# Performance work log

Measured on AMD Instinct MI355X. Metric: run time of the kernel, lower is better.

## Reference

```python
import jax, jax.numpy as jnp
import numpy as np
from jax import lax

N_ANT = 16
T_SNAP = 512
M_SRC = 3
BATCH = 1024
N_ANGLES = 360


def setup_inputs() -> dict:
    key = jax.random.key(0)
    ks = jax.random.split(key, 16)
    H = 2 * N_ANT  # GRU input/hidden size
    p = lambda k, shp, s=0.05: jax.random.normal(k, shp, jnp.float32) * s
    return {
        "X_real": jax.random.normal(ks[0], (BATCH, N_ANT, T_SNAP), jnp.float32),
        "X_imag": jax.random.normal(ks[1], (BATCH, N_ANT, T_SNAP), jnp.float32),
        "bn_w": jnp.ones((T_SNAP,), jnp.float32),
        "bn_b": jnp.zeros((T_SNAP,), jnp.float32),
        "gru_Wih": p(ks[2], (3 * H, H), 0.1),
        "gru_Whh": p(ks[3], (3 * H, H), 0.1),
        "gru_bih": p(ks[4], (3 * H,), 0.1),
        "gru_bhh": p(ks[5], (3 * H,), 0.1),
        "fc_W": p(ks[6], (H * N_ANT, H)),
        "fc_b": p(ks[7], (H * N_ANT,)),
        "fc1_W": p(ks[8], (H, N_ANGLES)),
        "fc1_b": p(ks[9], (H,)),
        "fc2_W": p(ks[10], (H, H)),
        "fc2_b": p(ks[11], (H,)),
        "fc3_W": p(ks[12], (M_SRC, H)),
        "fc3_b": p(ks[13], (M_SRC,)),
    }


def _gru_last(x, Wih, Whh, bih, bhh):
    # x: [B, T, I]; torch GRU gate order: r, z, n. Returns last hidden state [B, H].
    B = x.shape[0]
    H = Whh.shape[1]

    def step(h, xt):
        gi = xt @ Wih.T + bih
        gh = h @ Whh.T + bhh
        ir, iz, inn = jnp.split(gi, 3, axis=-1)
        hr, hz, hn = jnp.split(gh, 3, axis=-1)
        r = jax.nn.sigmoid(ir + hr)
        z = jax.nn.sigmoid(iz + hz)
        n = jnp.tanh(inn + r * hn)
        h_new = (1.0 - z) * n + z * h
        return h_new, None

    h0 = jnp.zeros((B, H), x.dtype)
    hT, _ = lax.scan(step, h0, jnp.swapaxes(x, 0, 1))
    return hT


def reference(X_real, X_imag, bn_w, bn_b, gru_Wih, gru_Whh, gru_bih, gru_bhh,
              fc_W, fc_b, fc1_W, fc1_b, fc2_W, fc2_b, fc3_W, fc3_b):
    B, N, T = X_real.shape
    # cat(real, imag) on antenna dim -> [B, 2N, T], then raw view to [B, T, 2N] (faithful to .view)
    X = jnp.concatenate([X_real, X_imag], axis=1).reshape(B, T, 2 * N)
    # BatchNorm1d(T): channel dim is axis 1, training-mode batch stats (biased var), eps=1e-5
    mean = X.mean(axis=(0, 2), keepdims=True)
    var = ((X - mean) ** 2).mean(axis=(0, 2), keepdims=True)
    X = (X - mean) / jnp.sqrt(var + 1e-5) * bn_w[None, :, None] + bn_b[None, :, None]
    # GRU -> last hidden -> fc -> [B, 2N, N] -> complex N x N correlation matrix
    h = _gru_last(X, gru_Wih, gru_Whh, gru_bih, gru_bhh)
    Rx = (h @ fc_W.T + fc_b).reshape(B, 2 * N, N)
    K = lax.complex(Rx[:, :N, :], Rx[:, N:, :])  # [B, N, N] complex64
    # batched general eigendecomposition; sort by |eigval| descending, keep noise subspace
    w, V = jnp.linalg.eig(K)
    order = jnp.flip(jnp.argsort(jnp.abs(w), axis=-1), axis=-1)
    Vs = jnp.take_along_axis(V, order[:, None, :], axis=2)
    Un = Vs[:, :, M_SRC:]  # [B, N, N-M]
    # MUSIC pseudo-spectrum over all 360 angles in one einsum
    angles = jnp.linspace(-np.pi / 2, np.pi / 2, N_ANGLES).astype(jnp.float32)
    phase = np.pi * jnp.arange(N, dtype=jnp.float32)[None, :] * jnp.sin(angles)[:, None]
    A = jnp.exp(lax.complex(jnp.zeros_like(phase), -phase))  # [360, N], a = exp(-j*pi*k*sin(theta))
    s = jnp.einsum('an,bnk->bak', jnp.conj(A), Un)  # a^H @ Un
    denom = jnp.sum(jnp.real(s) ** 2 + jnp.imag(s) ** 2, axis=-1)  # a^H Un Un^H a (real, >=0)
    spectrum = 1.0 / denom  # [B, 360]
    # MLP head (fc2 applied twice, as in the original)
    y = jax.nn.relu(spectrum @ fc1_W.T + fc1_b)
    y = jax.nn.relu(y @ fc2_W.T + fc2_b)
    y = jax.nn.relu(y @ fc2_W.T + fc2_b)
    return y @ fc3_W.T + fc3_b  # DOA: [B, M]
```

## Files before the change

### kernel.cpp

```cpp
#include <hip/hip_runtime.h>

#define PI_D 3.14159265358979323846
#define BATCH 1024
#define NOISE_K 13
#define N_ANGLES 360

#define WS_BNA    0
#define WS_BNB    (WS_BNA + 512)
#define WS_H      (WS_BNB + 512)
#define WS_RX     (WS_H + BATCH*32)
#define WS_CA     (WS_RX + BATCH*512)
#define WS_FC1T   (WS_CA + N_ANGLES*16*2)
#define WS_UN     (WS_FC1T + N_ANGLES*32)

__device__ __forceinline__ float2 f2(float a, float b){ return make_float2(a,b); }
__device__ __forceinline__ float2 fadd2(float2 a, float2 b){ return f2(a.x+b.x, a.y+b.y); }
__device__ __forceinline__ float2 fsub2(float2 a, float2 b){ return f2(a.x-b.x, a.y-b.y); }
__device__ __forceinline__ float2 fmul2(float2 a, float2 b){ return f2(a.x*b.x - a.y*b.y, a.x*b.y + a.y*b.x); }
__device__ __forceinline__ float2 fconj2(float2 a){ return f2(a.x, -a.y); }
__device__ __forceinline__ float2 fscale2(float2 a, float s){ return f2(a.x*s, a.y*s); }
__device__ __forceinline__ float  fabs2sq(float2 a){ return a.x*a.x + a.y*a.y; }
__device__ __forceinline__ float2 fmad2(float2 b, float2 c, float2 a){ return fadd2(a, fmul2(b,c)); }
__device__ __forceinline__ float2 fdivc2(float2 a, float2 b){
  float id = __frcp_rn(b.x*b.x + b.y*b.y);
  return f2((a.x*b.x + a.y*b.y)*id, (a.y*b.x - a.x*b.y)*id);
}
__device__ __forceinline__ float2 csqrtf2(float2 z){
  float m = __fsqrt_rn(z.x*z.x + z.y*z.y);
  if (m == 0.f) return f2(0.f, 0.f);
  float u = __fsqrt_rn(0.5f*(m + fabsf(z.x)));
  if (z.x >= 0.f) return f2(u, z.y/(2.f*u));
  float v = (z.y >= 0.f) ? u : -u;
  return f2(z.y/(2.f*v), v);
}

__global__ void prep_kernel(const float* __restrict__ fc1W, float* __restrict__ CA,
                            float* __restrict__ fc1T){
  int i = blockIdx.x*256 + threadIdx.x;
  if (i < N_ANGLES*16){
    int a = i >> 4, n = i & 15;
    float ang = (float)(-PI_D*0.5 + (double)a * (PI_D/359.0));
    float ph = (float)PI_D * (float)n * sinf(ang);
    CA[2*i]   = cosf(ph);
    CA[2*i+1] = sinf(ph);
  }
  if (i < N_ANGLES*32){
    int a = i >> 5, j = i & 31;
    fc1T[i] = fc1W[j*N_ANGLES + a];
  }
}

__global__ __launch_bounds__(256) void bn_stats_kernel(
    const float* __restrict__ Xr, const float* __restrict__ Xi,
    const float* __restrict__ bnw, const float* __restrict__ bnb,
    float* __restrict__ bnA, float* __restrict__ bnB){
  const int tp = blockIdx.x;
  const int n = tp >> 4;
  const float* src = (n < 16) ? Xr : Xi;
  const size_t roff = (size_t)(n & 15)*512 + (size_t)(tp & 15)*32;
  const int c4 = threadIdx.x & 7;
  const int bg = threadIdx.x >> 3;
  double s = 0.0, ss = 0.0;
  for (int i = 0; i < 32; i++){
    int b = bg*32 + i;
    const float4 v = *(const float4*)(src + (size_t)b*8192 + roff + c4*4);
    s  += (double)v.x + (double)v.y + (double)v.z + (double)v.w;
    ss += (double)v.x*v.x + (double)v.y*v.y + (double)v.z*v.z + (double)v.w*v.w;
  }
  for (int m=1; m<64; m<<=1){ s += __shfl_xor(s, m, 64); ss += __shfl_xor(ss, m, 64); }
  __shared__ double sh[4][2];
  int wid = threadIdx.x >> 6, lane = threadIdx.x & 63;
  if (lane == 0){ sh[wid][0] = s; sh[wid][1] = ss; }
  __syncthreads();
  if (threadIdx.x == 0){
    double S  = sh[0][0]+sh[1][0]+sh[2][0]+sh[3][0];
    double SS = sh[0][1]+sh[1][1]+sh[2][1]+sh[3][1];
    double mean = S/32768.0;
    double var  = SS/32768.0 - mean*mean;
    double inv  = 1.0/sqrt(var + 1e-5);
    double a = (double)bnw[tp]*inv;
    bnA[tp] = (float)a;
    bnB[tp] = (float)((double)bnb[tp] - mean*a);
  }
}

__global__ __launch_bounds__(256) void gru_kernel(
    const float* __restrict__ Xr, const float* __restrict__ Xi,
    const float* __restrict__ Wih, const float* __restrict__ Whh,
    const float* __restrict__ bih, const float* __restrict__ bhh,
    const float* __restrict__ bnA, const float* __restrict__ bnB,
    float* __restrict__ hbuf){
  const int lane = threadIdx.x & 63;
  const int wv   = threadIdx.x >> 6;
  const int b    = blockIdx.x*4 + wv;
  const int j    = lane & 31;
  const int k0   = (lane >> 5)*16;
  const int tt0  = lane >> 3;
  __shared__ float xb[4][2][512];
  __shared__ float hl[4][32];

  float WI0[16], WI1[16], WI2[16], WH0[16], WH1[16], WH2[16];
  #pragma unroll
  for (int kk=0; kk<16; kk++){
    WI0[kk] = Wih[(j     )*32 + k0+kk];
    WI1[kk] = Wih[(32+j  )*32 + k0+kk];
    WI2[kk] = Wih[(64+j  )*32 + k0+kk];
    WH0[kk] = Whh[(j     )*32 + k0+kk];
    WH1[kk] = Whh[(32+j  )*32 + k0+kk];
    WH2[kk] = Whh[(64+j  )*32 + k0+kk];
  }
  const float br  = bih[j]    + bhh[j];
  const float bz  = bih[32+j] + bhh[32+j];
  const float bin = bih[64+j];
  const float bhn = bhh[64+j];
  const size_t xbase = (size_t)b*8192;

  {
    const float* s0 = Xr + xbase;
    float4 p0 = *(const float4*)(s0 + lane*4);
    float4 p1 = *(const float4*)(s0 + 256 + lane*4);
    const float a0 = bnA[tt0],   b0 = bnB[tt0];
    const float a1 = bnA[8+tt0], b1 = bnB[8+tt0];
    p0.x = fmaf(p0.x,a0,b0); p0.y = fmaf(p0.y,a0,b0); p0.z = fmaf(p0.z,a0,b0); p0.w = fmaf(p0.w,a0,b0);
    p1.x = fmaf(p1.x,a1,b1); p1.y = fmaf(p1.y,a1,b1); p1.z = fmaf(p1.z,a1,b1); p1.w = fmaf(p1.w,a1,b1);
    *(float4*)&xb[wv][0][lane*4]       = p0;
    *(float4*)&xb[wv][0][256 + lane*4] = p1;
  }
  hl[wv][j] = 0.f;
  float h = 0.f;

  for (int m=0; m<32; m++){
    float4 q0, q1; float a0n=0.f,b0n=0.f,a1n=0.f,b1n=0.f;
    if (m < 31){
      const int mm = m+1;
      const float* s2 = ((mm < 16) ? Xr : Xi) + xbase + (size_t)(mm & 15)*512;
      q0 = *(const float4*)(s2 + lane*4);
      q1 = *(const float4*)(s2 + 256 + lane*4);
      a0n = bnA[mm*16+tt0];   b0n = bnB[mm*16+tt0];
      a1n = bnA[mm*16+8+tt0]; b1n = bnB[mm*16+8+tt0];
    }
    const float* xc = xb[wv][m & 1];
    for (int tt=0; tt<16; tt++){
      const float4 ha = *(const float4*)&hl[wv][k0];
      const float4 hb = *(const float4*)&hl[wv][k0 + 4];
      const float4 hc = *(const float4*)&hl[wv][k0 + 8];
      const float4 hd = *(const float4*)&hl[wv][k0 + 12];
      const float4 xa = *(const float4*)&xc[tt*32 + k0];
      const float4 xb2= *(const float4*)&xc[tt*32 + k0 + 4];
      const float4 xc2= *(const float4*)&xc[tt*32 + k0 + 8];
      const float4 xd = *(const float4*)&xc[tt*32 + k0 + 12];
      float xr16[16] = {xa.x,xa.y,xa.z,xa.w, xb2.x,xb2.y,xb2.z,xb2.w,
                        xc2.x,xc2.y,xc2.z,xc2.w, xd.x,xd.y,xd.z,xd.w};
      float gxr=0.f, gxz=0.f, gxn=0.f;
      #pragma unroll
      for (int kk=0; kk<16; kk++){
        gxr = fmaf(xr16[kk], WI0[kk], gxr);
        gxz = fmaf(xr16[kk], WI1[kk], gxz);
        gxn = fmaf(xr16[kk], WI2[kk], gxn);
      }
      float hr16[16] = {ha.x,ha.y,ha.z,ha.w, hb.x,hb.y,hb.z,hb.w,
                        hc.x,hc.y,hc.z,hc.w, hd.x,hd.y,hd.z,hd.w};
      float ghr=0.f, ghz=0.f, ghn=0.f;
      #pragma unroll
      for (int kk=0; kk<16; kk++){
        ghr = fmaf(hr16[kk], WH0[kk], ghr);
        ghz = fmaf(hr16[kk], WH1[kk], ghz);
        ghn = fmaf(hr16[kk], WH2[kk], ghn);
      }
      float grt = gxr + ghr;
      float gzt = gxz + ghz;
      grt += __shfl_xor(grt, 32, 64);
      gzt += __shfl_xor(gzt, 32, 64);
      float gnx = gxn + __shfl_xor(gxn, 32, 64);
      float hnv = ghn + __shfl_xor(ghn, 32, 64);
      const float r = __frcp_rn(1.0f + __expf(-(grt + br)));
      const float z = __frcp_rn(1.0f + __expf(-(gzt + bz)));
      const float nn = gnx + bin + r*(hnv + bhn);
      const float th = 1.0f - 2.0f*__frcp_rn(1.0f + __expf(2.0f*nn));
      h = th + z*(h - th);
      hl[wv][j] = h;
    }
    if (m < 31){
      q0.x = fmaf(q0.x,a0n,b0n); q0.y = fmaf(q0.y,a0n,b0n); q0.z = fmaf(q0.z,a0n,b0n); q0.w = fmaf(q0.w,a0n,b0n);
      q1.x = fmaf(q1.x,a1n,b1n); q1.y = fmaf(q1.y,a1n,b1n); q1.z = fmaf(q1.z,a1n,b1n); q1.w = fmaf(q1.w,a1n,b1n);
      *(float4*)&xb[wv][(m+1)&1][lane*4]       = q0;
      *(float4*)&xb[wv][(m+1)&1][256 + lane*4] = q1;
    }
  }
  if (lane < 32) hbuf[(size_t)b*32 + j] = h;
}

__global__ __launch_bounds__(256) void rx_kernel(
    const float* __restrict__ hbuf, const float* __restrict__ fcW,
    const float* __restrict__ fcb, float* __restrict__ Rx){
  const int b = blockIdx.x;
  __shared__ float hs[32];
  if (threadIdx.x < 32) hs[threadIdx.x] = hbuf[(size_t)b*32 + threadIdx.x];
  __syncthreads();
  for (int o = threadIdx.x; o < 512; o += 256){
    float acc = fcb[o];
    const float4* W4 = (const float4*)(fcW + o*32);
    const float4* H4 = (const float4*)hs;
    #pragma unroll
    for (int q=0; q<8; q++){
      const float4 w = W4[q], hh = H4[q];
      acc += w.x*hh.x + w.y*hh.y + w.z*hh.z + w.w*hh.w;
    }
    Rx[(size_t)b*512 + o] = acc;
  }
}

#define LD 17
__global__ __launch_bounds__(64) void eig_kernel(
    const float* __restrict__ Rx, float* __restrict__ Un){
  __shared__ float2 T[16*LD];
  __shared__ float2 Q[16*LD];
  __shared__ float2 Y[16*LD];
  __shared__ float2 ev[16];
  const int lane = threadIdx.x;
  const int b = blockIdx.x;
  const float* rx = Rx + (size_t)b*512;

  float hn2;
  {
    const float4 re = *(const float4*)(rx + lane*4);
    const float4 im = *(const float4*)(rx + 256 + lane*4);
    const float rr[4] = {re.x, re.y, re.z, re.w};
    const float ii[4] = {im.x, im.y, im.z, im.w};
    #pragma unroll
    for (int q=0; q<4; q++){
      const int e = lane*4 + q;
      const int r = e >> 4, c = e & 15;
      T[r*LD+c] = f2(rr[q], ii[q]);
      Q[r*LD+c] = f2((r==c)?1.f:0.f, 0.f);
    }
    float hp = rr[0]*rr[0]+rr[1]*rr[1]+rr[2]*rr[2]+rr[3]*rr[3]
             + ii[0]*ii[0]+ii[1]*ii[1]+ii[2]*ii[2]+ii[3]*ii[3];
    for (int m=1; m<64; m<<=1) hp += __shfl_xor(hp, m, 64);
    hn2 = (hp == 0.f) ? 1.f : hp;
  }
  __builtin_amdgcn_wave_barrier();

  for (int k=0; k<14; k++){
    float2 xr = f2(0.f,0.f);
    if (lane >= k+1 && lane < 16) xr = T[lane*LD+k];
    float nx2 = fabs2sq(xr);
    nx2 += __shfl_xor(nx2, 1, 64);
    nx2 += __shfl_xor(nx2, 2, 64);
    nx2 += __shfl_xor(nx2, 4, 64);
    nx2 += __shfl_xor(nx2, 8, 64);
    nx2 = __shfl(nx2, lane & 15, 64);
    if (nx2 > 1e-30f){
      const float2 alpha = T[(k+1)*LD+k];
      const float anorm = __fsqrt_rn(fabs2sq(alpha));
      const float normx = __fsqrt_rn(nx2);
      const float2 beta = (anorm > 0.f) ? fscale2(alpha, -normx/anorm) : f2(-normx, 0.f);
      const float vn2 = 2.f*nx2 + 2.f*normx*anorm;
      const float inv = __frsqrt_rn(vn2);
      float2 wvl = fscale2(xr, inv);
      if (lane == k+1) wvl = fscale2(fsub2(xr, beta), inv);
      if (lane < 16) ev[lane] = (lane >= k+1) ? wvl : f2(0.f,0.f);
      __builtin_amdgcn_wave_barrier();
      if (lane < 16){
        float2 d = f2(0.f,0.f);
        for (int r=k+1; r<16; r++) d = fmad2(fconj2(ev[r]), T[r*LD+lane], d);
        d = fscale2(d, 2.f);
        for (int r=k+1; r<16; r++) T[r*LD+lane] = fsub2(T[r*LD+lane], fmul2(ev[r], d));
      }
      __builtin_amdgcn_wave_barrier();
      if (lane < 32){
        const int r0 = lane & 15;
        float2* M = (lane < 16) ? T : Q;
        float2 d = f2(0.f,0.f);
        for (int r=k+1; r<16; r++) d = fmad2(M[r0*LD+r], ev[r], d);
        d = fscale2(d, 2.f);
        for (int r=k+1; r<16; r++) M[r0*LD+r] = fsub2(M[r0*LD+r], fmul2(d, fconj2(ev[r])));
      }
      __builtin_amdgcn_wave_barrier();
    }
  }

  unsigned long long deflmask = 0ull;
  int hi = 15, its = 0;
  const float eps2f = 1e-9f;
  for (int tot=0; tot<96; tot++){
    float2 sub = f2(0.f,0.f), dd0 = f2(0.f,0.f), dd1 = f2(0.f,0.f);
    if (lane >= 1 && lane < 16){
      sub = T[lane*LD+lane-1];
      dd0 = T[(lane-1)*LD+(lane-1)];
      dd1 = T[lane*LD+lane];
    }
    float sc2 = fabs2sq(dd0) + fabs2sq(dd1);
    if (sc2 == 0.f) sc2 = hn2;
    const bool fdef = (lane >= 1 && lane < 16) && (fabs2sq(sub) <= eps2f*sc2);
    deflmask |= __ballot(fdef);
    while (hi > 0 && ((deflmask >> hi) & 1ull)){ hi--; its = 0; }
    if (hi <= 0) break;
    const unsigned long long m2 = deflmask & ((1ull << hi) - 1ull);
    const int lo = m2 ? (63 - __builtin_clzll(m2)) : 0;
    its++;
    const float2 aa = T[(hi-1)*LD+hi-1];
    const float2 bb = T[(hi-1)*LD+hi];
    const float2 cc = T[hi*LD+hi-1];
    const float2 dd = T[hi*LD+hi];
    const float2 x0 = T[lo*LD+lo];
    const float2 y0 = T[(lo+1)*LD+lo];
    float2 mu;
    if (its % 5 == 0){
      mu = f2(dd.x + 0.75f*__fsqrt_rn(fabs2sq(cc)), dd.y);
    } else {
      const float2 t2 = fscale2(fsub2(aa, dd), 0.5f);
      const float2 bc = fmul2(bb, cc);
      const float2 del = csqrtf2(fadd2(fmul2(t2, t2), bc));
      const float2 d1 = fadd2(t2, del), d2v = fsub2(t2, del);
      const float2 den = (fabs2sq(d1) >= fabs2sq(d2v)) ? d1 : d2v;
      mu = (fabs2sq(den) > 0.f) ? fsub2(dd, fdivc2(bc, den)) : dd;
    }
    float2 x = fsub2(x0, mu);
    float2 y = y0;
    for (int i=lo; i<hi; i++){
      const float ax2 = fabs2sq(x), ay2 = fabs2sq(y);
      float c_; float2 s;
      if (ax2 < 1e-30f){
        if (ay2 < 1e-37f){ c_ = 1.f; s = f2(0.f,0.f); }
        else { c_ = 0.f; s = fscale2(fconj2(y), __frsqrt_rn(ay2)); }
      } else {
        const float inv_ax = __frsqrt_rn(ax2);
        const float inv_rr = __frsqrt_rn(ax2 + ay2);
        c_ = ax2*inv_ax*inv_rr;
        s = fscale2(fmul2(x, fconj2(y)), inv_ax*inv_rr);
      }
      const int q16 = lane & 15;
      const int role = lane >> 4;
      float2* Mp = (role == 2) ? Q : T;
      int ia = 0, ib = 0; bool active = false;
      if (role == 0){ ia = i*LD+q16; ib = (i+1)*LD+q16; active = (q16!=i)&&(q16!=i+1); }
      else if (role == 1){ ia = q16*LD+i; ib = ia+1; active = (q16!=i)&&(q16!=i+1); }
      else if (role == 2){ ia = q16*LD+i; ib = ia+1; active = true; }
      if (active){
        const float2 A = Mp[ia], B = Mp[ib];
        const float2 sl = (role == 0) ? s : fconj2(s);
        Mp[ia] = fadd2(fscale2(A, c_), fmul2(sl, B));
        Mp[ib] = fsub2(fscale2(B, c_), fmul2(fconj2(sl), A));
      }
      if (role == 3 && q16 < 4){
        const float2 t00 = T[i*LD+i],     t01 = T[i*LD+i+1];
        const float2 t10 = T[(i+1)*LD+i], t11 = T[(i+1)*LD+i+1];
        const float2 r0c0 = fadd2(fscale2(t00, c_), fmul2(s, t10));
        const float2 r0c1 = fadd2(fscale2(t01, c_), fmul2(s, t11));
        const float2 r1c0 = fsub2(fscale2(t10, c_), fmul2(fconj2(s), t00));
        const float2 r1c1 = fsub2(fscale2(t11, c_), fmul2(fconj2(s), t01));
        float2 outv;
        if (q16 == 0)      outv = fadd2(fscale2(r0c0, c_), fmul2(fconj2(s), r0c1));
        else if (q16 == 1) outv = fsub2(fscale2(r0c1, c_), fmul2(s, r0c0));
        else if (q16 == 2) outv = fadd2(fscale2(r1c0, c_), fmul2(fconj2(s), r1c1));
        else               outv = fsub2(fscale2(r1c1, c_), fmul2(s, r1c0));
        T[(i+(q16>>1))*LD + (i+(q16&1))] = outv;
      }
      __builtin_amdgcn_wave_barrier();
      if (i < hi-1){
        x = T[(i+1)*LD+i];
        y = T[(i+2)*LD+i];
      }
    }
  }
  __builtin_amdgcn_wave_barrier();

  if (lane < 16) ev[lane] = T[lane*LD+lane];
  __builtin_amdgcn_wave_barrier();
  const float hnf = __fsqrt_rn(hn2);
  const float smin = 1e-6f*hnf + 1e-35f;
  if (lane < 16){
    const int i = lane;
    const float2 lam = ev[i];
    Y[i*LD+i] = f2(1.f, 0.f);
    for (int jj=i-1; jj>=0; jj--){
      float2 sum = f2(0.f,0.f);
      for (int k2=jj+1; k2<=i; k2++) sum = fmad2(T[jj*LD+k2], Y[k2*LD+i], sum);
      float2 den = fsub2(T[jj*LD+jj], lam);
      if (fabs2sq(den) < smin*smin) den = f2(smin, 0.f);
      Y[jj*LD+i] = fdivc2(f2(-sum.x, -sum.y), den);
    }
  }
  __builtin_amdgcn_wave_barrier();
  {
    const int i = lane & 15;
    const int g = lane >> 4;
    float2 v[4]; float nrm = 0.f;
    #pragma unroll
    for (int q=0; q<4; q++){
      const int n = 4*g + q;
      float2 acc = f2(0.f,0.f);
      for (int k2=0; k2<=i; k2++) acc = fmad2(Q[n*LD+k2], Y[k2*LD+i], acc);
      v[q] = acc; nrm += fabs2sq(acc);
    }
    nrm += __shfl_xor(nrm, 16, 64);
    nrm += __shfl_xor(nrm, 32, 64);
    const float inv = __frsqrt_rn(nrm);
    const float mi = fabs2sq(ev[i]);
    int rank = 0;
    for (int k2=0; k2<16; k2++){
      const float mk = fabs2sq(ev[k2]);
      rank += (mk > mi) || (mk == mi && k2 > i);
    }
    if (rank >= 3){
      float* dst = Un + ((size_t)b*NOISE_K + (rank-3))*32 + 8*g;
      float4 w0, w1;
      w0.x = v[0].x*inv; w0.y = v[0].y*inv;
      w0.z = v[1].x*inv; w0.w = v[1].y*inv;
      w1.x = v[2].x*inv; w1.y = v[2].y*inv;
      w1.z = v[3].x*inv; w1.w = v[3].y*inv;
      ((float4*)dst)[0] = w0;
      ((float4*)dst)[1] = w1;
    }
  }
}

__global__ __launch_bounds__(256) void spec_head_kernel(
    const float* __restrict__ Un, const float* __restrict__ CA,
    const float* __restrict__ fc1T, const float* __restrict__ fc1b,
    const float* __restrict__ fc2W, const float* __restrict__ fc2b,
    const float* __restrict__ fc3W, const float* __restrict__ fc3b,
    float* __restrict__ out){
  const int b = blockIdx.x;
  const int tid = threadIdx.x;
  __shared__ float2 Us[NOISE_K*16];
  __shared__ float spec[N_ANGLES];
  __shared__ float y1[32], y2[32];
  if (tid < NOISE_K*16) Us[tid] = ((const float2*)Un)[(size_t)b*NOISE_K*16 + tid];
  __syncthreads();
  for (int a = tid; a < N_ANGLES; a += 256){
    float sr[NOISE_K], si[NOISE_K];
    #pragma unroll
    for (int k=0; k<NOISE_K; k++){ sr[k]=0.f; si[k]=0.f; }
    for (int n=0; n<16; n++){
      float2 ca = ((const float2*)CA)[a*16+n];
      #pragma unroll
      for (int k=0; k<NOISE_K; k++){
        float2 u = Us[k*16+n];
        sr[k] += ca.x*u.x - ca.y*u.y;
        si[k] += ca.x*u.y + ca.y*u.x;
      }
    }
    float d = 0.f;
    #pragma unroll
    for (int k=0; k<NOISE_K; k++) d += sr[k]*sr[k] + si[k]*si[k];
    spec[a] = 1.0f/d;
  }
  __syncthreads();
  if (tid < 32){
    float acc = fc1b[tid];
    for (int a=0; a<N_ANGLES; a++) acc += spec[a]*fc1T[a*32+tid];
    y1[tid] = fmaxf(acc, 0.f);
  }
  __syncthreads();
  if (tid < 32){
    float acc = fc2b[tid];
    #pragma unroll
    for (int k=0; k<32; k++) acc += y1[k]*fc2W[tid*32+k];
    y2[tid] = fmaxf(acc, 0.f);
  }
  __syncthreads();
  if (tid < 32){
    float acc = fc2b[tid];
    #pragma unroll
    for (int k=0; k<32; k++) acc += y2[k]*fc2W[tid*32+k];
    y1[tid] = fmaxf(acc, 0.f);
  }
  __syncthreads();
  if (tid < 3){
    float acc = fc3b[tid];
    #pragma unroll
    for (int k=0; k<32; k++) acc += y1[k]*fc3W[tid*32+k];
    out[(size_t)b*3 + tid] = acc;
  }
}

extern "C" void kernel_launch(void* const* d_in, const int* in_sizes, int n_in,
                              void* d_out, int out_size, void* d_ws, size_t ws_size,
                              hipStream_t stream){
  (void)in_sizes; (void)n_in; (void)out_size; (void)ws_size;
  const float* Xr   = (const float*)d_in[0];
  const float* Xi   = (const float*)d_in[1];
  const float* bnw  = (const float*)d_in[2];
  const float* bnb  = (const float*)d_in[3];
  const float* Wih  = (const float*)d_in[4];
  const float* Whh  = (const float*)d_in[5];
  const float* bih  = (const float*)d_in[6];
  const float* bhh  = (const float*)d_in[7];
  const float* fcW  = (const float*)d_in[8];
  const float* fcb  = (const float*)d_in[9];
  const float* fc1W = (const float*)d_in[10];
  const float* fc1b = (const float*)d_in[11];
  const float* fc2W = (const float*)d_in[12];
  const float* fc2b = (const float*)d_in[13];
  const float* fc3W = (const float*)d_in[14];
  const float* fc3b = (const float*)d_in[15];

  float* ws   = (float*)d_ws;
  float* bnA  = ws + WS_BNA;
  float* bnB  = ws + WS_BNB;
  float* hbuf = ws + WS_H;
  float* RxB  = ws + WS_RX;
  float* CA   = ws + WS_CA;
  float* fc1T = ws + WS_FC1T;
  float* UnB  = ws + WS_UN;

  hipLaunchKernelGGL(prep_kernel, dim3(45), dim3(256), 0, stream, fc1W, CA, fc1T);
  hipLaunchKernelGGL(bn_stats_kernel, dim3(512), dim3(256), 0, stream,
                     Xr, Xi, bnw, bnb, bnA, bnB);
  hipLaunchKernelGGL(gru_kernel, dim3(256), dim3(256), 0, stream,
                     Xr, Xi, Wih, Whh, bih, bhh, bnA, bnB, hbuf);
  hipLaunchKernelGGL(rx_kernel, dim3(1024), dim3(256), 0, stream,
                     hbuf, fcW, fcb, RxB);
  hipLaunchKernelGGL(eig_kernel, dim3(1024), dim3(64), 0, stream, RxB, UnB);
  hipLaunchKernelGGL(spec_head_kernel, dim3(1024), dim3(256), 0, stream,
                     UnB, CA, fc1T, fc1b, fc2W, fc2b, fc3W, fc3b, (float*)d_out);
}
```

Measured before the change: 894.0 us.

## Software-pipeline GRU input loads and cap QR eigen iteration count

Result: no change. 879.0 us (-1.7%).

```diff
diff --git a/kernel.cpp b/kernel.cpp
--- a/kernel.cpp
+++ b/kernel.cpp
@@ -126,37 +126,74 @@
     *(float4*)&xb[wv][0][lane*4]       = p0;
     *(float4*)&xb[wv][0][256 + lane*4] = p1;
   }
+  float4 q0, q1; float a0n, b0n, a1n, b1n;
+  {
+    const float* s1 = Xr + xbase + 512;
+    q0 = *(const float4*)(s1 + lane*4);
+    q1 = *(const float4*)(s1 + 256 + lane*4);
+    a0n = bnA[16+tt0]; b0n = bnB[16+tt0];
+    a1n = bnA[24+tt0]; b1n = bnB[24+tt0];
+  }
   hl[wv][j] = 0.f;
   float h = 0.f;
+  float xcur[16];
+  {
+    const float4 xa = *(const float4*)&xb[wv][0][k0];
+    const float4 xbv= *(const float4*)&xb[wv][0][k0+4];
+    const float4 xc2= *(const float4*)&xb[wv][0][k0+8];
+    const float4 xd = *(const float4*)&xb[wv][0][k0+12];
+    xcur[0]=xa.x; xcur[1]=xa.y; xcur[2]=xa.z; xcur[3]=xa.w;
+    xcur[4]=xbv.x; xcur[5]=xbv.y; xcur[6]=xbv.z; xcur[7]=xbv.w;
+    xcur[8]=xc2.x; xcur[9]=xc2.y; xcur[10]=xc2.z; xcur[11]=xc2.w;
+    xcur[12]=xd.x; xcur[13]=xd.y; xcur[14]=xd.z; xcur[15]=xd.w;
+  }
 
   for (int m=0; m<32; m++){
-    float4 q0, q1; float a0n=0.f,b0n=0.f,a1n=0.f,b1n=0.f;
+    const float* xc = xb[wv][m & 1];
+    float* xn = xb[wv][(m+1) & 1];
     if (m < 31){
-      const int mm = m+1;
+      q0.x = fmaf(q0.x,a0n,b0n); q0.y = fmaf(q0.y,a0n,b0n); q0.z = fmaf(q0.z,a0n,b0n); q0.w = fmaf(q0.w,a0n,b0n);
+      q1.x = fmaf(q1.x,a1n,b1n); q1.y = fmaf(q1.y,a1n,b1n); q1.z = fmaf(q1.z,a1n,b1n); q1.w = fmaf(q1.w,a1n,b1n);
+      *(float4*)&xn[lane*4]       = q0;
+      *(float4*)&xn[256 + lane*4] = q1;
+    }
+    if (m < 30){
+      const int mm = m+2;
       const float* s2 = ((mm < 16) ? Xr : Xi) + xbase + (size_t)(mm & 15)*512;
       q0 = *(const float4*)(s2 + lane*4);
       q1 = *(const float4*)(s2 + 256 + lane*4);
       a0n = bnA[mm*16+tt0];   b0n = bnB[mm*16+tt0];
       a1n = bnA[mm*16+8+tt0]; b1n = bnB[mm*16+8+tt0];
     }
-    const float* xc = xb[wv][m & 1];
+    #pragma unroll
     for (int tt=0; tt<16; tt++){
       const float4 ha = *(const float4*)&hl[wv][k0];
       const float4 hb = *(const float4*)&hl[wv][k0 + 4];
       const float4 hc = *(const float4*)&hl[wv][k0 + 8];
       const float4 hd = *(const float4*)&hl[wv][k0 + 12];
-      const float4 xa = *(const float4*)&xc[tt*32 + k0];
-      const float4 xb2= *(const float4*)&xc[tt*32 + k0 + 4];
-      const float4 xc2= *(const float4*)&xc[tt*32 + k0 + 8];
-      const float4 xd = *(const float4*)&xc[tt*32 + k0 + 12];
-      float xr16[16] = {xa.x,xa.y,xa.z,xa.w, xb2.x,xb2.y,xb2.z,xb2.w,
-                        xc2.x,xc2.y,xc2.z,xc2.w, xd.x,xd.y,xd.z,xd.w};
+      const bool last = (tt == 15);
+      const float* xsrc = last ? xn : xc;
+      const int xoff = last ? k0 : (tt+1)*32 + k0;
+      float xnext[16];
+      if (!last || m < 31){
+        const float4 na = *(const float4*)&xsrc[xoff];
+        const float4 nb = *(const float4*)&xsrc[xoff+4];
+        const float4 nc = *(const float4*)&xsrc[xoff+8];
+        const float4 nd = *(const float4*)&xsrc[xoff+12];
+        xnext[0]=na.x; xnext[1]=na.y; xnext[2]=na.z; xnext[3]=na.w;
+        xnext[4]=nb.x; xnext[5]=nb.y; xnext[6]=nb.z; xnext[7]=nb.w;
+        xnext[8]=nc.x; xnext[9]=nc.y; xnext[10]=nc.z; xnext[11]=nc.w;
+        xnext[12]=nd.x; xnext[13]=nd.y; xnext[14]=nd.z; xnext[15]=nd.w;
+      } else {
+        #pragma unroll
+        for (int kk=0; kk<16; kk++) xnext[kk] = 0.f;
+      }
       float gxr=0.f, gxz=0.f, gxn=0.f;
       #pragma unroll
       for (int kk=0; kk<16; kk++){
-        gxr = fmaf(xr16[kk], WI0[kk], gxr);
-        gxz = fmaf(xr16[kk], WI1[kk], gxz);
-        gxn = fmaf(xr16[kk], WI2[kk], gxn);
+        gxr = fmaf(xcur[kk], WI0[kk], gxr);
+        gxz = fmaf(xcur[kk], WI1[kk], gxz);
+        gxn = fmaf(xcur[kk], WI2[kk], gxn);
       }
       float hr16[16] = {ha.x,ha.y,ha.z,ha.w, hb.x,hb.y,hb.z,hb.w,
                         hc.x,hc.y,hc.z,hc.w, hd.x,hd.y,hd.z,hd.w};
@@ -179,12 +216,8 @@
       const float th = 1.0f - 2.0f*__frcp_rn(1.0f + __expf(2.0f*nn));
       h = th + z*(h - th);
       hl[wv][j] = h;
-    }
-    if (m < 31){
-      q0.x = fmaf(q0.x,a0n,b0n); q0.y = fmaf(q0.y,a0n,b0n); q0.z = fmaf(q0.z,a0n,b0n); q0.w = fmaf(q0.w,a0n,b0n);
-      q1.x = fmaf(q1.x,a1n,b1n); q1.y = fmaf(q1.y,a1n,b1n); q1.z = fmaf(q1.z,a1n,b1n); q1.w = fmaf(q1.w,a1n,b1n);
-      *(float4*)&xb[wv][(m+1)&1][lane*4]       = q0;
-      *(float4*)&xb[wv][(m+1)&1][256 + lane*4] = q1;
+      #pragma unroll
+      for (int kk=0; kk<16; kk++) xcur[kk] = xnext[kk];
     }
   }
   if (lane < 32) hbuf[(size_t)b*32 + j] = h;
@@ -283,7 +316,7 @@
   unsigned long long deflmask = 0ull;
   int hi = 15, its = 0;
   const float eps2f = 1e-9f;
-  for (int tot=0; tot<96; tot++){
+  for (int tot=0; tot<72; tot++){
     float2 sub = f2(0.f,0.f), dd0 = f2(0.f,0.f), dd1 = f2(0.f,0.f);
     if (lane >= 1 && lane < 16){
       sub = T[lane*LD+lane-1];
```
